# Performance work log

Hardware: AMD Instinct MI355X
Metric: run time of the kernel (lower is better)

## Reference

```python
import jax, jax.numpy as jnp
import numpy as np

NHEAD = 16


def setup_inputs() -> dict:
    key = jax.random.key(0)
    ks = jax.random.split(key, 6)
    S, B, D = 2048, 2, 1024
    std = float(np.sqrt(6.0 / (D + D)))  # xavier_uniform bound
    inp = {
        "query": jax.random.normal(ks[0], (S, B, D), jnp.float32),
        "key": jax.random.normal(ks[1], (S, B, D), jnp.float32),
        "value": jax.random.normal(ks[2], (S, B, D), jnp.float32),
        "Wq": jax.random.uniform(ks[3], (D, D), jnp.float32, -std, std),
        "bq": jnp.ones((D,), jnp.float32),
        "Wk": jax.random.uniform(ks[4], (D, D), jnp.float32, -std, std),
        "bk": jnp.ones((D,), jnp.float32),
        "Wv": jax.random.uniform(ks[5], (D, D), jnp.float32, -std, std),
        "bv": jnp.ones((D,), jnp.float32),
    }
    return inp


def reference(query, key, value, Wq, bq, Wk, bk, Wv, bv):
    S, B, D = query.shape
    h = NHEAD
    d = D // h
    scale = jnp.asarray(d ** 0.5, query.dtype)
    # projections (nn.Linear: x @ W^T + b)
    q = (query @ Wq.T + bq).reshape(S, B, h, d)
    k = (key @ Wk.T + bk).reshape(S, B, h, d)
    v = (value @ Wv.T + bv).reshape(S, B, h, d)
    # batch_first=False path: scores [b,h,i,j], softmax over j, then AV
    scores = jnp.einsum('ibhd,jbhd->bhij', q, k) / scale
    attn = jax.nn.softmax(scores, axis=-1)
    out = jnp.einsum('bhij,jbhd->ibhd', attn, v).reshape(S, B, D)
    return out
```

## Files before the change

kernel.cpp:

```cpp
#include <hip/hip_runtime.h>
#include <hip/hip_bf16.h>

#define S_LEN 2048
#define BATCH 2
#define DMODEL 1024
#define NHEAD 16
#define HDIM 64
#define MTOT (S_LEN * BATCH)
#define QKV_ELEMS ((size_t)MTOT * DMODEL)

typedef __bf16 bf16x8 __attribute__((ext_vector_type(8)));
typedef unsigned short u16x8 __attribute__((ext_vector_type(8)));
typedef float f32x4 __attribute__((ext_vector_type(4)));
typedef float f32x16 __attribute__((ext_vector_type(16)));
typedef unsigned int u32x4 __attribute__((ext_vector_type(4)));

__device__ __forceinline__ unsigned short f2bf(float f) {
    unsigned int u = __float_as_uint(f);
    u += 0x7FFFu + ((u >> 16) & 1u);
    return (unsigned short)(u >> 16);
}

__device__ __forceinline__ void gload_lds16(const void* g, void* l) {
    __builtin_amdgcn_global_load_lds(
        (const __attribute__((address_space(1))) unsigned int*)g,
        (__attribute__((address_space(3))) unsigned int*)l, 16, 0, 0);
}

#define PBM 128
#define PBN 128
#define PBK 32
#define PLDS 48
#define QSCALE 0.18033688011112042f

__global__ __launch_bounds__(256) void proj_kernel(
        const float* __restrict__ Xq, const float* __restrict__ Xk,
        const float* __restrict__ Xv, const float* __restrict__ Wq,
        const float* __restrict__ Wk, const float* __restrict__ Wv,
        const float* __restrict__ bq, const float* __restrict__ bk,
        const float* __restrict__ bv, unsigned short* __restrict__ ws)
{
    const int work = (blockIdx.x & 7) * 96 + (blockIdx.x >> 3);
    const int t    = work >> 8;
    const int rem  = work & 255;
    const int m0   = (rem >> 3) * PBM;
    const int n0   = (rem & 7) * PBN;

    const float* X    = (t == 0) ? Xq : (t == 1) ? Xk : Xv;
    const float* W    = (t == 0) ? Wq : (t == 1) ? Wk : Wv;
    const float* bias = (t == 0) ? bq : (t == 1) ? bk : bv;
    unsigned short* out = ws + (size_t)t * QKV_ELEMS;
    const float scale = (t == 0) ? QSCALE : 1.0f;

    __shared__ __align__(16) unsigned short lds[(PBM + PBN) * PLDS];
    unsigned short* Alds = lds;
    unsigned short* Blds = lds + PBM * PLDS;

    const int tid = threadIdx.x;
    const int wave = tid >> 6;
    const int lane = tid & 63;
    const int lrow = lane & 15;
    const int lg   = lane >> 4;
    const int wr = (wave >> 1) * 64;
    const int wc = (wave & 1) * 64;

    f32x4 acc[4][4];
#pragma unroll
    for (int i = 0; i < 4; ++i)
#pragma unroll
        for (int j = 0; j < 4; ++j)
            acc[i][j] = (f32x4){0.f, 0.f, 0.f, 0.f};

    const int sr = tid >> 3;
    const int sg = tid & 7;

    for (int k0 = 0; k0 < DMODEL; k0 += PBK) {
        __syncthreads();
#pragma unroll
        for (int it = 0; it < 4; ++it) {
            const int row = sr + it * 32;
            const float4 va = *(const float4*)(X + (size_t)(m0 + row) * DMODEL + k0 + sg * 4);
            const float4 vb = *(const float4*)(W + (size_t)(n0 + row) * DMODEL + k0 + sg * 4);
            ushort4 ha, hb;
            ha.x = f2bf(va.x); ha.y = f2bf(va.y); ha.z = f2bf(va.z); ha.w = f2bf(va.w);
            hb.x = f2bf(vb.x); hb.y = f2bf(vb.y); hb.z = f2bf(vb.z); hb.w = f2bf(vb.w);
            *(ushort4*)&Alds[row * PLDS + sg * 4] = ha;
            *(ushort4*)&Blds[row * PLDS + sg * 4] = hb;
        }
        __syncthreads();

        bf16x8 af[4], bw[4];
#pragma unroll
        for (int i = 0; i < 4; ++i) {
            af[i] = *(const bf16x8*)&Alds[(wr + i * 16 + lrow) * PLDS + lg * 8];
            bw[i] = *(const bf16x8*)&Blds[(wc + i * 16 + lrow) * PLDS + lg * 8];
        }
#pragma unroll
        for (int i = 0; i < 4; ++i)
#pragma unroll
            for (int j = 0; j < 4; ++j)
                acc[i][j] = __builtin_amdgcn_mfma_f32_16x16x32_bf16(af[i], bw[j], acc[i][j], 0, 0, 0);
    }

#pragma unroll
    for (int j = 0; j < 4; ++j) {
        const int n  = n0 + wc + j * 16 + lrow;
        const float bv_ = bias[n];
        const int h  = n >> 6;
        const int dd = n & 63;
#pragma unroll
        for (int i = 0; i < 4; ++i) {
#pragma unroll
            for (int r = 0; r < 4; ++r) {
                const int m = m0 + wr + i * 16 + lg * 4 + r;
                const int s = m >> 1;
                const int b = m & 1;
                const float v = (acc[i][j][r] + bv_) * scale;
                size_t idx;
                if (t == 2)
                    idx = ((size_t)((b * NHEAD + h) * HDIM + dd)) * S_LEN + s;
                else
                    idx = ((size_t)((b * NHEAD + h) * S_LEN + s)) * HDIM + dd;
                out[idx] = f2bf(v);
            }
        }
    }
}

#define NT (S_LEN / 64)

__global__ __launch_bounds__(512) void attn_kernel(
        const unsigned short* __restrict__ ws, float* __restrict__ out)
{
    const unsigned short* Qw = ws;
    const unsigned short* Kw = ws + QKV_ELEMS;
    const unsigned short* Vw = ws + 2 * QKV_ELEMS;

    const int bid = blockIdx.x;
    const int idx = bid >> 3;
    const int bh  = (bid & 7) * 4 + (idx >> 3);
    const int q0  = (idx & 7) * 256;

    __shared__ __align__(16) unsigned short Kbuf[2][64 * 64];
    __shared__ __align__(16) unsigned short Vbuf[2][64 * 64];
    __shared__ unsigned int Pu[8][32 * 32];

    const int tid  = threadIdx.x;
    const int wave = tid >> 6;
    const int lane = tid & 63;
    const int l31  = lane & 31;
    const int half = lane >> 5;

    const size_t base = (size_t)bh * S_LEN * HDIM;
    const int qrow = q0 + wave * 32 + l31;

    bf16x8 qf[4];
#pragma unroll
    for (int c = 0; c < 4; ++c)
        qf[c] = *(const bf16x8*)(Qw + base + (size_t)qrow * HDIM + c * 16 + half * 8);

    f32x16 Od0, Od1;
#pragma unroll
    for (int i = 0; i < 16; ++i) { Od0[i] = 0.f; Od1[i] = 0.f; }
    float mrun = -__builtin_inff();
    float lrun = 0.f;

    const int srow = tid >> 3;
    const int sgrp = (tid & 7) ^ (srow & 7);
    const int dsto = tid * 8;

    gload_lds16(Kw + base + (size_t)srow * HDIM + sgrp * 8,  &Kbuf[0][dsto]);
    gload_lds16(Vw + base + (size_t)srow * S_LEN + sgrp * 8, &Vbuf[0][dsto]);
    __syncthreads();

    int cur = 0;
    for (int t = 0; t < NT; ++t) {
        if (t + 1 < NT) {
            const int sn = (t + 1) * 64;
            gload_lds16(Kw + base + (size_t)(sn + srow) * HDIM + sgrp * 8, &Kbuf[cur ^ 1][dsto]);
            gload_lds16(Vw + base + (size_t)srow * S_LEN + sn + sgrp * 8, &Vbuf[cur ^ 1][dsto]);
        }

        const unsigned short* Klds = Kbuf[cur];
        const unsigned short* Vlds = Vbuf[cur];

        f32x16 S0, S1;
#pragma unroll
        for (int i = 0; i < 16; ++i) { S0[i] = 0.f; S1[i] = 0.f; }
        __builtin_amdgcn_s_setprio(1);
#pragma unroll
        for (int c = 0; c < 4; ++c) {
            const int g = ((c * 2 + half) ^ (l31 & 7)) * 8;
            const bf16x8 ka0 = *(const bf16x8*)&Klds[l31 * 64 + g];
            const bf16x8 ka1 = *(const bf16x8*)&Klds[(32 + l31) * 64 + g];
            S0 = __builtin_amdgcn_mfma_f32_32x32x16_bf16(ka0, qf[c], S0, 0, 0, 0);
            S1 = __builtin_amdgcn_mfma_f32_32x32x16_bf16(ka1, qf[c], S1, 0, 0, 0);
        }
        __builtin_amdgcn_s_setprio(0);

        f32x16 mx16;
#pragma unroll
        for (int i = 0; i < 16; ++i) mx16[i] = fmaxf(S0[i], S1[i]);
        float m8[8], m4[4], m2[2];
#pragma unroll
        for (int i = 0; i < 8; ++i) m8[i] = fmaxf(mx16[i], mx16[i + 8]);
#pragma unroll
        for (int i = 0; i < 4; ++i) m4[i] = fmaxf(m8[i], m8[i + 4]);
        m2[0] = fmaxf(m4[0], m4[2]); m2[1] = fmaxf(m4[1], m4[3]);
        float mx = fmaxf(m2[0], m2[1]);
        mx = fmaxf(mx, __shfl_xor(mx, 32, 64));

        if (!__all(mx - mrun <= 8.0f)) {
            const float mnew = fmaxf(mrun, mx);
            const float ex   = exp2f(mrun - mnew);
            mrun = mnew;
            lrun *= ex;
            Od0 *= ex;
            Od1 *= ex;
        }

#pragma unroll
        for (int i = 0; i < 16; ++i) S0[i] = exp2f(S0[i] - mrun);
#pragma unroll
        for (int i = 0; i < 16; ++i) S1[i] = exp2f(S1[i] - mrun);
        f32x16 sv = S0 + S1;
        float s8[8], s4[4];
#pragma unroll
        for (int i = 0; i < 8; ++i) s8[i] = sv[i] + sv[i + 8];
#pragma unroll
        for (int i = 0; i < 4; ++i) s4[i] = s8[i] + s8[i + 4];
        float psum = (s4[0] + s4[2]) + (s4[1] + s4[3]);
        psum += __shfl_xor(psum, 32, 64);
        lrun += psum;

#pragma unroll
        for (int w = 0; w < 8; ++w) {
            const unsigned int pk0 = (unsigned int)f2bf(S0[2 * w])
                                   | ((unsigned int)f2bf(S0[2 * w + 1]) << 16);
            const unsigned int pk1 = (unsigned int)f2bf(S1[2 * w])
                                   | ((unsigned int)f2bf(S1[2 * w + 1]) << 16);
            const int kp = (w & 1) + 4 * (w >> 1) + 2 * half;
            Pu[wave][kp * 32 + l31]        = pk0;
            Pu[wave][(16 + kp) * 32 + l31] = pk1;
        }
        __asm__ volatile("" ::: "memory");

        __builtin_amdgcn_s_setprio(1);
#pragma unroll
        for (int c = 0; c < 4; ++c) {
            const int g = ((c * 2 + half) ^ (l31 & 7)) * 8;
            const bf16x8 va0 = *(const bf16x8*)&Vlds[l31 * 64 + g];
            const bf16x8 va1 = *(const bf16x8*)&Vlds[(32 + l31) * 64 + g];
            u32x4 pu;
#pragma unroll
            for (int e = 0; e < 4; ++e)
                pu[e] = Pu[wave][(c * 8 + half * 4 + e) * 32 + l31];
            const bf16x8 pb = __builtin_bit_cast(bf16x8, pu);
            Od0 = __builtin_amdgcn_mfma_f32_32x32x16_bf16(va0, pb, Od0, 0, 0, 0);
            Od1 = __builtin_amdgcn_mfma_f32_32x32x16_bf16(va1, pb, Od1, 0, 0, 0);
        }
        __builtin_amdgcn_s_setprio(0);

        __syncthreads();
        cur ^= 1;
    }

    const int bb = bh >> 4;
    const int hh = bh & 15;
    const float inv = 1.0f / lrun;
    float* op = out + (size_t)qrow * (BATCH * DMODEL) + bb * DMODEL + hh * HDIM;
#pragma unroll
    for (int gg = 0; gg < 4; ++gg) {
        const int d0 = gg * 8 + half * 4;
        float4 v0, v1;
        v0.x = Od0[gg * 4 + 0] * inv; v0.y = Od0[gg * 4 + 1] * inv;
        v0.z = Od0[gg * 4 + 2] * inv; v0.w = Od0[gg * 4 + 3] * inv;
        v1.x = Od1[gg * 4 + 0] * inv; v1.y = Od1[gg * 4 + 1] * inv;
        v1.z = Od1[gg * 4 + 2] * inv; v1.w = Od1[gg * 4 + 3] * inv;
        *(float4*)(op + d0)      = v0;
        *(float4*)(op + 32 + d0) = v1;
    }
}

extern "C" void kernel_launch(void* const* d_in, const int* in_sizes, int n_in,
                              void* d_out, int out_size, void* d_ws, size_t ws_size,
                              hipStream_t stream) {
    const float* q  = (const float*)d_in[0];
    const float* k  = (const float*)d_in[1];
    const float* v  = (const float*)d_in[2];
    const float* Wq = (const float*)d_in[3];
    const float* bq = (const float*)d_in[4];
    const float* Wk = (const float*)d_in[5];
    const float* bk = (const float*)d_in[6];
    const float* Wv = (const float*)d_in[7];
    const float* bv = (const float*)d_in[8];
    unsigned short* ws = (unsigned short*)d_ws;
    float* out = (float*)d_out;

    proj_kernel<<<dim3(768), dim3(256), 0, stream>>>(q, k, v, Wq, Wk, Wv, bq, bk, bv, ws);
    attn_kernel<<<dim3(256), dim3(512), 0, stream>>>(ws, out);
}
```

Baseline: 153.2 us.

## Compute softmax row sums via MFMA with ones vector, use packed bf16 convert

Replaces the VALU reduction tree and cross-lane shuffle for the softmax denominator with an extra MFMA that multiplies a vector of ones by the bf16 probability tile. It also switches to a hardware packed float2-to-bf16 conversion, hoists the swizzle offsets out of the loop, and reshapes the max reduction into three-operand steps. This offloads VALU work to the matrix unit, but adds a third MFMA per chunk and 16 more accumulator registers. The denominator is now summed from the bf16-rounded probabilities, which slightly changes numerics and may lower occupancy.

```diff
diff --git a/kernel.cpp b/kernel.cpp
--- a/kernel.cpp
+++ b/kernel.cpp
@@ -19,6 +19,13 @@
     unsigned int u = __float_as_uint(f);
     u += 0x7FFFu + ((u >> 16) & 1u);
     return (unsigned short)(u >> 16);
+}
+
+__device__ __forceinline__ unsigned int pack2(float lo, float hi) {
+    __hip_bfloat162 h = __float22bfloat162_rn(make_float2(lo, hi));
+    unsigned int r;
+    __builtin_memcpy(&r, &h, 4);
+    return r;
 }
 
 __device__ __forceinline__ void gload_lds16(const void* g, void* l) {
@@ -159,11 +166,22 @@
     for (int c = 0; c < 4; ++c)
         qf[c] = *(const bf16x8*)(Qw + base + (size_t)qrow * HDIM + c * 16 + half * 8);
 
-    f32x16 Od0, Od1;
-#pragma unroll
-    for (int i = 0; i < 16; ++i) { Od0[i] = 0.f; Od1[i] = 0.f; }
+    bf16x8 ones;
+    {
+        u16x8 o;
+#pragma unroll
+        for (int e = 0; e < 8; ++e) o[e] = 0x3F80;
+        ones = __builtin_bit_cast(bf16x8, o);
+    }
+
+    f32x16 Od0, Od1, Lacc;
+#pragma unroll
+    for (int i = 0; i < 16; ++i) { Od0[i] = 0.f; Od1[i] = 0.f; Lacc[i] = 0.f; }
     float mrun = -__builtin_inff();
-    float lrun = 0.f;
+
+    int g_[4];
+#pragma unroll
+    for (int c = 0; c < 4; ++c) g_[c] = ((c * 2 + half) ^ (l31 & 7)) * 8;
 
     const int srow = tid >> 3;
     const int sgrp = (tid & 7) ^ (srow & 7);
@@ -190,55 +208,44 @@
         __builtin_amdgcn_s_setprio(1);
 #pragma unroll
         for (int c = 0; c < 4; ++c) {
-            const int g = ((c * 2 + half) ^ (l31 & 7)) * 8;
-            const bf16x8 ka0 = *(const bf16x8*)&Klds[l31 * 64 + g];
-            const bf16x8 ka1 = *(const bf16x8*)&Klds[(32 + l31) * 64 + g];
+            const bf16x8 ka0 = *(const bf16x8*)&Klds[l31 * 64 + g_[c]];
+            const bf16x8 ka1 = *(const bf16x8*)&Klds[(32 + l31) * 64 + g_[c]];
             S0 = __builtin_amdgcn_mfma_f32_32x32x16_bf16(ka0, qf[c], S0, 0, 0, 0);
             S1 = __builtin_amdgcn_mfma_f32_32x32x16_bf16(ka1, qf[c], S1, 0, 0, 0);
         }
         __builtin_amdgcn_s_setprio(0);
 
-        f32x16 mx16;
-#pragma unroll
-        for (int i = 0; i < 16; ++i) mx16[i] = fmaxf(S0[i], S1[i]);
-        float m8[8], m4[4], m2[2];
-#pragma unroll
-        for (int i = 0; i < 8; ++i) m8[i] = fmaxf(mx16[i], mx16[i + 8]);
-#pragma unroll
-        for (int i = 0; i < 4; ++i) m4[i] = fmaxf(m8[i], m8[i + 4]);
-        m2[0] = fmaxf(m4[0], m4[2]); m2[1] = fmaxf(m4[1], m4[3]);
-        float mx = fmaxf(m2[0], m2[1]);
+        float m16[16];
+#pragma unroll
+        for (int i = 0; i < 16; ++i) m16[i] = fmaxf(S0[i], S1[i]);
+        float a0 = fmaxf(fmaxf(m16[0],  m16[1]),  m16[2]);
+        float a1 = fmaxf(fmaxf(m16[3],  m16[4]),  m16[5]);
+        float a2 = fmaxf(fmaxf(m16[6],  m16[7]),  m16[8]);
+        float a3 = fmaxf(fmaxf(m16[9],  m16[10]), m16[11]);
+        float a4 = fmaxf(fmaxf(m16[12], m16[13]), m16[14]);
+        float b0 = fmaxf(fmaxf(a0, a1), a2);
+        float b1 = fmaxf(fmaxf(a3, a4), m16[15]);
+        float mx = fmaxf(b0, b1);
         mx = fmaxf(mx, __shfl_xor(mx, 32, 64));
 
         if (!__all(mx - mrun <= 8.0f)) {
             const float mnew = fmaxf(mrun, mx);
             const float ex   = exp2f(mrun - mnew);
             mrun = mnew;
-            lrun *= ex;
             Od0 *= ex;
             Od1 *= ex;
+            Lacc *= ex;
         }
 
 #pragma unroll
         for (int i = 0; i < 16; ++i) S0[i] = exp2f(S0[i] - mrun);
 #pragma unroll
         for (int i = 0; i < 16; ++i) S1[i] = exp2f(S1[i] - mrun);
-        f32x16 sv = S0 + S1;
-        float s8[8], s4[4];
-#pragma unroll
-        for (int i = 0; i < 8; ++i) s8[i] = sv[i] + sv[i + 8];
-#pragma unroll
-        for (int i = 0; i < 4; ++i) s4[i] = s8[i] + s8[i + 4];
-        float psum = (s4[0] + s4[2]) + (s4[1] + s4[3]);
-        psum += __shfl_xor(psum, 32, 64);
-        lrun += psum;
 
 #pragma unroll
         for (int w = 0; w < 8; ++w) {
-            const unsigned int pk0 = (unsigned int)f2bf(S0[2 * w])
-                                   | ((unsigned int)f2bf(S0[2 * w + 1]) << 16);
-            const unsigned int pk1 = (unsigned int)f2bf(S1[2 * w])
-                                   | ((unsigned int)f2bf(S1[2 * w + 1]) << 16);
+            const unsigned int pk0 = pack2(S0[2 * w], S0[2 * w + 1]);
+            const unsigned int pk1 = pack2(S1[2 * w], S1[2 * w + 1]);
             const int kp = (w & 1) + 4 * (w >> 1) + 2 * half;
             Pu[wave][kp * 32 + l31]        = pk0;
             Pu[wave][(16 + kp) * 32 + l31] = pk1;
@@ -248,16 +255,16 @@
         __builtin_amdgcn_s_setprio(1);
 #pragma unroll
         for (int c = 0; c < 4; ++c) {
-            const int g = ((c * 2 + half) ^ (l31 & 7)) * 8;
-            const bf16x8 va0 = *(const bf16x8*)&Vlds[l31 * 64 + g];
-            const bf16x8 va1 = *(const bf16x8*)&Vlds[(32 + l31) * 64 + g];
+            const bf16x8 va0 = *(const bf16x8*)&Vlds[l31 * 64 + g_[c]];
+            const bf16x8 va1 = *(const bf16x8*)&Vlds[(32 + l31) * 64 + g_[c]];
             u32x4 pu;
 #pragma unroll
             for (int e = 0; e < 4; ++e)
                 pu[e] = Pu[wave][(c * 8 + half * 4 + e) * 32 + l31];
             const bf16x8 pb = __builtin_bit_cast(bf16x8, pu);
-            Od0 = __builtin_amdgcn_mfma_f32_32x32x16_bf16(va0, pb, Od0, 0, 0, 0);
-            Od1 = __builtin_amdgcn_mfma_f32_32x32x16_bf16(va1, pb, Od1, 0, 0, 0);
+            Od0  = __builtin_amdgcn_mfma_f32_32x32x16_bf16(va0,  pb, Od0,  0, 0, 0);
+            Od1  = __builtin_amdgcn_mfma_f32_32x32x16_bf16(va1,  pb, Od1,  0, 0, 0);
+            Lacc = __builtin_amdgcn_mfma_f32_32x32x16_bf16(ones, pb, Lacc, 0, 0, 0);
         }
         __builtin_amdgcn_s_setprio(0);
 
@@ -267,7 +274,7 @@
 
     const int bb = bh >> 4;
     const int hh = bh & 15;
-    const float inv = 1.0f / lrun;
+    const float inv = 1.0f / Lacc[0];
     float* op = out + (size_t)qrow * (BATCH * DMODEL) + bb * DMODEL + hh * HDIM;
 #pragma unroll
     for (int gg = 0; gg < 4; ++gg) {
```

Result: no change. 151.1 us (-1.3%).
